# Kernel optimization log

Measured on AMD Instinct MI355X. Metric: run time of the kernel, lower is better.

Reference implementation:

```python
import jax, jax.numpy as jnp
import numpy as np

NUM_HEADS = 12


def setup_inputs() -> dict:
    key = jax.random.key(0)
    ks = jax.random.split(key, 6)
    dim = 384
    B, N = 2048, 49
    nW = 64
    return {
        "x": jax.random.normal(ks[0], (B, N, dim), dtype=jnp.float32),
        "mask": jax.random.normal(ks[1], (nW, N, N), dtype=jnp.float32),
        "qkv_w": jax.random.normal(ks[2], (3 * dim, dim), dtype=jnp.float32) * 0.02,
        "qkv_b": jax.random.normal(ks[3], (3 * dim,), dtype=jnp.float32) * 0.02,
        "proj_w": jax.random.normal(ks[4], (dim, dim), dtype=jnp.float32) * 0.02,
        "proj_b": jax.random.normal(ks[5], (dim,), dtype=jnp.float32) * 0.02,
    }


def reference(x, mask, qkv_w, qkv_b, proj_w, proj_b):
    B, N, C = x.shape
    H = NUM_HEADS
    Dh = C // H
    scale = Dh ** -0.5
    nW = mask.shape[0]

    # qkv projection: [B, N, 3C]
    qkv = x @ qkv_w.T + qkv_b
    q, k, v = jnp.split(qkv, 3, axis=-1)

    def heads(t):  # [B, N, C] -> [B, H, N, Dh]
        return t.reshape(B, N, H, Dh).transpose(0, 2, 1, 3)

    q, k, v = heads(q) * scale, heads(k), heads(v)

    # [B, H, N, N] attention scores
    attn = jnp.einsum("bhnd,bhmd->bhnm", q, k)
    # add per-window additive mask: reshape B -> (B//nW, nW)
    attn = attn.reshape(B // nW, nW, H, N, N) + mask[None, :, None, :, :]
    attn = jax.nn.softmax(attn.reshape(B, H, N, N), axis=-1)

    out = jnp.einsum("bhnm,bhmd->bhnd", attn, v)
    out = out.transpose(0, 2, 1, 3).reshape(B, N, C)
    return out @ proj_w.T + proj_b
```

## Files before the change

### kernel.cpp

```cpp
#include <hip/hip_runtime.h>
#include <hip/hip_bf16.h>
#include <stdint.h>

typedef unsigned short u16;
typedef __attribute__((ext_vector_type(8))) short short8;
typedef __attribute__((ext_vector_type(4))) short s4v;
typedef __attribute__((ext_vector_type(4))) float f32x4;

__device__ inline u16 f2bf(float f) {
    union { float f; unsigned int u; } x; x.f = f;
    unsigned int u = x.u;
    unsigned int r = (u + 0x7FFFu + ((u >> 16) & 1u)) >> 16;
    return (u16)r;
}

__device__ inline void gld_lds16(const u16* g, u16* l) {
    auto const* gp = reinterpret_cast<const __attribute__((address_space(1))) unsigned int*>(
        reinterpret_cast<uintptr_t>(g));
    auto* lp = reinterpret_cast<__attribute__((address_space(3))) unsigned int*>(
        reinterpret_cast<uintptr_t>(l));
    __builtin_amdgcn_global_load_lds(gp, lp, 16, 0, 0);
}

#if __has_builtin(__builtin_amdgcn_mfma_f32_16x16x16bf16_1k)
#define MFMA16(a, b, c) __builtin_amdgcn_mfma_f32_16x16x16bf16_1k((a), (b), (c), 0, 0, 0)
#elif __has_builtin(__builtin_amdgcn_mfma_f32_16x16x16_bf16)
#define MFMA16(a, b, c) __builtin_amdgcn_mfma_f32_16x16x16_bf16((a), (b), (c), 0, 0, 0)
#else
__device__ inline f32x4 mfma16_asm(s4v a, s4v b, f32x4 c) {
    asm volatile("s_nop 1\n\tv_mfma_f32_16x16x16_bf16 %0, %1, %2, %0\n\ts_nop 7\n\ts_nop 7"
                 : "+v"(c) : "v"(a), "v"(b));
    return c;
}
#define MFMA16(a, b, c) mfma16_asm((a), (b), (c))
#endif

#define NX8 4816896
#define NQ8 55296
#define NP8 18432
__global__ __launch_bounds__(256) void prep_all(const float* __restrict__ x,
                                                const float* __restrict__ qw,
                                                const float* __restrict__ pw,
                                                u16* __restrict__ xb,
                                                u16* __restrict__ wq,
                                                u16* __restrict__ wp) {
    size_t i = (size_t)blockIdx.x * 256 + threadIdx.x;
    const float* src; u16* dst; size_t off;
    if (i < NX8)            { src = x;  dst = xb; off = i; }
    else if (i < NX8 + NQ8) { src = qw; dst = wq; off = i - NX8; }
    else                    { src = pw; dst = wp; off = i - (NX8 + NQ8); }
    float4 v0 = ((const float4*)src)[off * 2];
    float4 v1 = ((const float4*)src)[off * 2 + 1];
    u16 h[8];
    h[0] = f2bf(v0.x); h[1] = f2bf(v0.y); h[2] = f2bf(v0.z); h[3] = f2bf(v0.w);
    h[4] = f2bf(v1.x); h[5] = f2bf(v1.y); h[6] = f2bf(v1.z); h[7] = f2bf(v1.w);
    *(uint4*)(dst + off * 8) = *(const uint4*)h;
}

__global__ __launch_bounds__(256) void qkv_gemm(const u16* __restrict__ xb,
                                                const u16* __restrict__ wq,
                                                const float* __restrict__ bias,
                                                u16* __restrict__ qkv_out) {
    __shared__ u16 As[2][128 * 32];
    __shared__ u16 Bs[2][128 * 32];
    const int tid = threadIdx.x;
    const int wave = tid >> 6, lane = tid & 63;
    const int lr = lane >> 4, lc = lane & 15;
    const int wm = (wave & 1) * 64, wn = (wave >> 1) * 64;
    const int lin = blockIdx.x;
    const int xcd = lin & 7;
    const int idx = lin >> 3;
    const int nBase = (idx % 9) * 128;
    const int mBase = (xcd * 98 + idx / 9) * 128;

    f32x4 acc[4][4] = {};

    const int srow = lane >> 2, scol = (lane & 3) * 8;
    const u16* aSrc = xb + (size_t)(mBase + wave * 32 + srow) * 384 + scol;
    const u16* bSrc = wq + (size_t)(nBase + wave * 32 + srow) * 384 + scol;

    auto stage = [&](int k0, int buf) {
        u16* aDst = &As[buf][wave * 1024];
        u16* bDst = &Bs[buf][wave * 1024];
        gld_lds16(aSrc + k0, aDst);
        gld_lds16(aSrc + k0 + (size_t)16 * 384, aDst + 512);
        gld_lds16(bSrc + k0, bDst);
        gld_lds16(bSrc + k0 + (size_t)16 * 384, bDst + 512);
    };
    auto compute = [&](int buf) {
        short8 af[4], bfr[4];
#pragma unroll
        for (int i = 0; i < 4; ++i)
            af[i] = *(const short8*)&As[buf][(wm + i * 16 + lc) * 32 + lr * 8];
#pragma unroll
        for (int j = 0; j < 4; ++j)
            bfr[j] = *(const short8*)&Bs[buf][(wn + j * 16 + lc) * 32 + lr * 8];
#pragma unroll
        for (int i = 0; i < 4; ++i)
#pragma unroll
            for (int j = 0; j < 4; ++j)
                acc[i][j] = __builtin_amdgcn_mfma_f32_16x16x32_bf16(bfr[j], af[i], acc[i][j], 0, 0, 0);
    };

    stage(0, 0);
    __syncthreads();
#pragma unroll
    for (int t = 0; t < 11; ++t) {
        stage((t + 1) * 32, (t + 1) & 1);
        compute(t & 1);
        __syncthreads();
    }
    compute(11 & 1);

    const float scale = 0.17677669529663687f;
#pragma unroll
    for (int j = 0; j < 4; ++j) {
        int gnb = nBase + wn + j * 16 + lr * 4;
        float4 bv = *(const float4*)&bias[gnb];
        float mult = (gnb < 384) ? scale : 1.0f;
#pragma unroll
        for (int i = 0; i < 4; ++i) {
            int gm = mBase + wm + i * 16 + lc;
            union { u16 h[4]; uint2 u; } pk;
            pk.h[0] = f2bf((acc[i][j][0] + bv.x) * mult);
            pk.h[1] = f2bf((acc[i][j][1] + bv.y) * mult);
            pk.h[2] = f2bf((acc[i][j][2] + bv.z) * mult);
            pk.h[3] = f2bf((acc[i][j][3] + bv.w) * mult);
            *(uint2*)(qkv_out + (size_t)gm * 1152 + gnb) = pk.u;
        }
    }
}

__global__ __launch_bounds__(256, 3) void attn_kernel(const u16* __restrict__ qkv,
                                                      const float* __restrict__ mask,
                                                      u16* __restrict__ aout) {
#define PST 68
    __shared__ u16 Vt_s[4][32 * PST];
    const int tid = threadIdx.x;
    const int wave = tid >> 6, lane = tid & 63;
    const int lr = lane >> 4, lc = lane & 15;
    const int bid = blockIdx.x;
    const int b = bid / 3;
    const int h = (bid - b * 3) * 4 + wave;
    const int w = b & 63;
    const float* mrow = mask + (size_t)w * 2401;

    const u16* Q = qkv + (size_t)b * 49 * 1152 + h * 32;
    const u16* K = Q + 384;
    const u16* V = Q + 768;

    {
        u16 vv[32];
        if (lane < 49) {
#pragma unroll
            for (int c = 0; c < 4; ++c)
                *(uint4*)&vv[c * 8] = *(const uint4*)(V + (size_t)lane * 1152 + c * 8);
        } else {
#pragma unroll
            for (int c = 0; c < 32; ++c) vv[c] = 0;
        }
#pragma unroll
        for (int d = 0; d < 32; ++d)
            Vt_s[wave][d * PST + lane] = vv[d];
    }

    short8 qf[4], kf[4];
    const short8 z8 = {0, 0, 0, 0, 0, 0, 0, 0};
#pragma unroll
    for (int i = 0; i < 4; ++i) {
        int row = i * 16 + lc;
        qf[i] = (row < 49) ? *(const short8*)(Q + (size_t)row * 1152 + lr * 8) : z8;
        kf[i] = (row < 49) ? *(const short8*)(K + (size_t)row * 1152 + lr * 8) : z8;
    }

    __syncthreads();

    s4v vfA[2][4];
#pragma unroll
    for (int nt = 0; nt < 2; ++nt)
#pragma unroll
        for (int sj = 0; sj < 4; ++sj)
            vfA[nt][sj] = *(const s4v*)&Vt_s[wave][(nt * 16 + lc) * PST + sj * 16 + lr * 4];

    f32x4 S2[4][4] = {};
#pragma unroll
    for (int si = 0; si < 4; ++si)
#pragma unroll
        for (int sj = 0; sj < 4; ++sj)
            S2[si][sj] = __builtin_amdgcn_mfma_f32_16x16x32_bf16(kf[sj], qf[si], S2[si][sj], 0, 0, 0);

    const size_t orow = (size_t)b * 49 * 384 + h * 32 + lr * 4;
#pragma unroll
    for (int si = 0; si < 4; ++si) {
        int q = si * 16 + lc;
        int im = (q < 49) ? q : 48;
        const float* mq = mrow + im * 49;
        float s = 0.0f;
        s4v pfq[4];
#pragma unroll
        for (int sj = 0; sj < 4; ++sj) {
            int kbase = sj * 16 + lr * 4;
            s4v pk;
#pragma unroll
            for (int r = 0; r < 4; ++r) {
                int k = kbase + r;
                float t = (k < 49) ? (S2[si][sj][r] + mq[k]) : -1e30f;
                float p = __expf(t);
                s += p;
                pk[r] = (short)f2bf(p);
            }
            pfq[sj] = pk;
        }
        s += __shfl_xor(s, 16);
        s += __shfl_xor(s, 32);

        f32x4 O0 = {}, O1 = {};
#pragma unroll
        for (int sj = 0; sj < 4; ++sj) {
            O0 = MFMA16(vfA[0][sj], pfq[sj], O0);
            O1 = MFMA16(vfA[1][sj], pfq[sj], O1);
        }

        if (q < 49) {
            float rl = __builtin_amdgcn_rcpf(s);
            union { u16 h[4]; uint2 u; } pk;
            pk.h[0] = f2bf(O0[0] * rl); pk.h[1] = f2bf(O0[1] * rl);
            pk.h[2] = f2bf(O0[2] * rl); pk.h[3] = f2bf(O0[3] * rl);
            *(uint2*)(aout + orow + (size_t)q * 384) = pk.u;
            pk.h[0] = f2bf(O1[0] * rl); pk.h[1] = f2bf(O1[1] * rl);
            pk.h[2] = f2bf(O1[2] * rl); pk.h[3] = f2bf(O1[3] * rl);
            *(uint2*)(aout + orow + (size_t)q * 384 + 16) = pk.u;
        }
    }
#undef PST
}

__global__ __launch_bounds__(256) void proj_gemm(const u16* __restrict__ a,
                                                 const u16* __restrict__ wp,
                                                 const float* __restrict__ bias,
                                                 float* __restrict__ out) {
    __shared__ u16 As[2][128 * 32];
    __shared__ u16 Bs[2][128 * 32];
    const int tid = threadIdx.x;
    const int wave = tid >> 6, lane = tid & 63;
    const int lr = lane >> 4, lc = lane & 15;
    const int wm = (wave & 1) * 64, wn = (wave >> 1) * 64;
    const int lin = blockIdx.x;
    const int xcd = lin & 7;
    const int idx = lin >> 3;
    const int nBase = (idx % 3) * 128;
    const int mBase = (xcd * 98 + idx / 3) * 128;

    f32x4 acc[4][4] = {};

    const int srow = lane >> 2, scol = (lane & 3) * 8;
    const u16* aSrc = a  + (size_t)(mBase + wave * 32 + srow) * 384 + scol;
    const u16* bSrc = wp + (size_t)(nBase + wave * 32 + srow) * 384 + scol;

    auto stage = [&](int k0, int buf) {
        u16* aDst = &As[buf][wave * 1024];
        u16* bDst = &Bs[buf][wave * 1024];
        gld_lds16(aSrc + k0, aDst);
        gld_lds16(aSrc + k0 + (size_t)16 * 384, aDst + 512);
        gld_lds16(bSrc + k0, bDst);
        gld_lds16(bSrc + k0 + (size_t)16 * 384, bDst + 512);
    };
    auto compute = [&](int buf) {
        short8 af[4], bfr[4];
#pragma unroll
        for (int i = 0; i < 4; ++i)
            af[i] = *(const short8*)&As[buf][(wm + i * 16 + lc) * 32 + lr * 8];
#pragma unroll
        for (int j = 0; j < 4; ++j)
            bfr[j] = *(const short8*)&Bs[buf][(wn + j * 16 + lc) * 32 + lr * 8];
#pragma unroll
        for (int i = 0; i < 4; ++i)
#pragma unroll
            for (int j = 0; j < 4; ++j)
                acc[i][j] = __builtin_amdgcn_mfma_f32_16x16x32_bf16(bfr[j], af[i], acc[i][j], 0, 0, 0);
    };

    stage(0, 0);
    __syncthreads();
#pragma unroll
    for (int t = 0; t < 11; ++t) {
        stage((t + 1) * 32, (t + 1) & 1);
        compute(t & 1);
        __syncthreads();
    }
    compute(11 & 1);

#pragma unroll
    for (int j = 0; j < 4; ++j) {
        int gnb = nBase + wn + j * 16 + lr * 4;
        float4 bv = *(const float4*)&bias[gnb];
#pragma unroll
        for (int i = 0; i < 4; ++i) {
            int gm = mBase + wm + i * 16 + lc;
            float4 o;
            o.x = acc[i][j][0] + bv.x;
            o.y = acc[i][j][1] + bv.y;
            o.z = acc[i][j][2] + bv.z;
            o.w = acc[i][j][3] + bv.w;
            *(float4*)(out + (size_t)gm * 384 + gnb) = o;
        }
    }
}

extern "C" void kernel_launch(void* const* d_in, const int* in_sizes, int n_in,
                              void* d_out, int out_size, void* d_ws, size_t ws_size,
                              hipStream_t stream) {
    const float* x      = (const float*)d_in[0];
    const float* mask   = (const float*)d_in[1];
    const float* qkv_w  = (const float*)d_in[2];
    const float* qkv_b  = (const float*)d_in[3];
    const float* proj_w = (const float*)d_in[4];
    const float* proj_b = (const float*)d_in[5];
    float* out = (float*)d_out;

    char* ws = (char*)d_ws;
    u16* wq   = (u16*)ws;
    u16* wp   = (u16*)(ws + 884736);
    u16* qkvb = (u16*)(ws + 1179648);
    u16* xb   = (u16*)(ws + 232390656);
    u16* attn = xb;

    prep_all<<<19104, 256, 0, stream>>>(x, qkv_w, proj_w, xb, wq, wp);
    qkv_gemm<<<7056, 256, 0, stream>>>(xb, wq, qkv_b, qkvb);
    attn_kernel<<<6144, 256, 0, stream>>>(qkvb, mask, attn);
    proj_gemm<<<2352, 256, 0, stream>>>(attn, wp, proj_b, out);
}
```

Before: 561.1 us.

## Fuse QKV projection and window attention into one kernel per head pair-window

Merges the QKV GEMM and the attention kernel. Each block computes Q, K and V for one head over two 49-row windows (98 rows) straight into LDS and then runs attention from LDS, so the bf16 qkv tensor never makes a round trip through global memory. The prep kernel reorders the QKV weight rows per head so each block loads a contiguous 96-row weight slice. The cost is a smaller 98-row M tile with clamped padding, six-way N fragments, and a larger LDS footprint per block.

Measured after the change: 509.2 us. 9.3% less time.

```diff
diff --git a/kernel.cpp b/kernel.cpp
--- a/kernel.cpp
+++ b/kernel.cpp
@@ -42,169 +42,164 @@
                                                 const float* __restrict__ qw,
                                                 const float* __restrict__ pw,
                                                 u16* __restrict__ xb,
-                                                u16* __restrict__ wq,
+                                                u16* __restrict__ wqr,
                                                 u16* __restrict__ wp) {
     size_t i = (size_t)blockIdx.x * 256 + threadIdx.x;
-    const float* src; u16* dst; size_t off;
-    if (i < NX8)            { src = x;  dst = xb; off = i; }
-    else if (i < NX8 + NQ8) { src = qw; dst = wq; off = i - NX8; }
-    else                    { src = pw; dst = wp; off = i - (NX8 + NQ8); }
-    float4 v0 = ((const float4*)src)[off * 2];
-    float4 v1 = ((const float4*)src)[off * 2 + 1];
+    const float* src; u16* dst; size_t soff, doff;
+    if (i < NX8) {
+        src = x; dst = xb; soff = i; doff = i;
+    } else if (i < NX8 + NQ8) {
+        size_t off = i - NX8;
+        int orow = (int)(off / 48);
+        int chunk = (int)(off - (size_t)orow * 48);
+        int sec = orow / 384;
+        int rem = orow - sec * 384;
+        int hh = rem >> 5, d = rem & 31;
+        int nrow = hh * 96 + sec * 32 + d;
+        src = qw; dst = wqr; soff = off; doff = (size_t)nrow * 48 + chunk;
+    } else {
+        src = pw; dst = wp; soff = i - (NX8 + NQ8); doff = soff;
+    }
+    float4 v0 = ((const float4*)src)[soff * 2];
+    float4 v1 = ((const float4*)src)[soff * 2 + 1];
     u16 h[8];
     h[0] = f2bf(v0.x); h[1] = f2bf(v0.y); h[2] = f2bf(v0.z); h[3] = f2bf(v0.w);
     h[4] = f2bf(v1.x); h[5] = f2bf(v1.y); h[6] = f2bf(v1.z); h[7] = f2bf(v1.w);
-    *(uint4*)(dst + off * 8) = *(const uint4*)h;
-}
-
-__global__ __launch_bounds__(256) void qkv_gemm(const u16* __restrict__ xb,
-                                                const u16* __restrict__ wq,
-                                                const float* __restrict__ bias,
-                                                u16* __restrict__ qkv_out) {
-    __shared__ u16 As[2][128 * 32];
-    __shared__ u16 Bs[2][128 * 32];
+    *(uint4*)(dst + doff * 8) = *(const uint4*)h;
+}
+
+__global__ __launch_bounds__(256, 3) void qkv_attn(const u16* __restrict__ xb,
+                                                   const u16* __restrict__ wqr,
+                                                   const float* __restrict__ bias,
+                                                   const float* __restrict__ mask,
+                                                   u16* __restrict__ aout) {
+    __shared__ __align__(16) u16 lds[14336];
+    u16* Abuf[2] = { lds, lds + 4096 };
+    u16* Bbuf[2] = { lds + 8192, lds + 11264 };
+    u16* QK = lds;
+    u16* Vt = lds + 8704;
+
     const int tid = threadIdx.x;
     const int wave = tid >> 6, lane = tid & 63;
     const int lr = lane >> 4, lc = lane & 15;
-    const int wm = (wave & 1) * 64, wn = (wave >> 1) * 64;
     const int lin = blockIdx.x;
     const int xcd = lin & 7;
     const int idx = lin >> 3;
-    const int nBase = (idx % 9) * 128;
-    const int mBase = (xcd * 98 + idx / 9) * 128;
-
-    f32x4 acc[4][4] = {};
+    const int h = idx % 12;
+    const int mp = xcd * 128 + idx / 12;
+    const int row0 = mp * 98;
+
+    f32x4 acc[2][6] = {};
 
     const int srow = lane >> 2, scol = (lane & 3) * 8;
-    const u16* aSrc = xb + (size_t)(mBase + wave * 32 + srow) * 384 + scol;
-    const u16* bSrc = wq + (size_t)(nBase + wave * 32 + srow) * 384 + scol;
+    const int ar0 = row0 + wave * 32 + srow;
+    const int ar1 = (ar0 < 100351) ? ar0 : 100351;
+    const int ar2 = (ar0 + 16 < 100351) ? ar0 + 16 : 100351;
+    const u16* aSrc1 = xb + (size_t)ar1 * 384 + scol;
+    const u16* aSrc2 = xb + (size_t)ar2 * 384 + scol;
+    const u16* bSrc = wqr + (size_t)(h * 96 + wave * 16 + srow) * 384 + scol;
 
     auto stage = [&](int k0, int buf) {
-        u16* aDst = &As[buf][wave * 1024];
-        u16* bDst = &Bs[buf][wave * 1024];
-        gld_lds16(aSrc + k0, aDst);
-        gld_lds16(aSrc + k0 + (size_t)16 * 384, aDst + 512);
-        gld_lds16(bSrc + k0, bDst);
-        gld_lds16(bSrc + k0 + (size_t)16 * 384, bDst + 512);
+        gld_lds16(aSrc1 + k0, Abuf[buf] + wave * 1024);
+        gld_lds16(aSrc2 + k0, Abuf[buf] + wave * 1024 + 512);
+        gld_lds16(bSrc + k0, Bbuf[buf] + wave * 512);
+        if (wave < 2)
+            gld_lds16(bSrc + (size_t)64 * 384 + k0, Bbuf[buf] + 2048 + wave * 512);
     };
     auto compute = [&](int buf) {
-        short8 af[4], bfr[4];
-#pragma unroll
-        for (int i = 0; i < 4; ++i)
-            af[i] = *(const short8*)&As[buf][(wm + i * 16 + lc) * 32 + lr * 8];
-#pragma unroll
-        for (int j = 0; j < 4; ++j)
-            bfr[j] = *(const short8*)&Bs[buf][(wn + j * 16 + lc) * 32 + lr * 8];
-#pragma unroll
-        for (int i = 0; i < 4; ++i)
-#pragma unroll
-            for (int j = 0; j < 4; ++j)
+        short8 af[2], bfr[6];
+#pragma unroll
+        for (int i = 0; i < 2; ++i)
+            af[i] = *(const short8*)&Abuf[buf][(wave * 32 + i * 16 + lc) * 32 + lr * 8];
+#pragma unroll
+        for (int j = 0; j < 6; ++j)
+            bfr[j] = *(const short8*)&Bbuf[buf][(j * 16 + lc) * 32 + lr * 8];
+#pragma unroll
+        for (int i = 0; i < 2; ++i)
+#pragma unroll
+            for (int j = 0; j < 6; ++j)
                 acc[i][j] = __builtin_amdgcn_mfma_f32_16x16x32_bf16(bfr[j], af[i], acc[i][j], 0, 0, 0);
     };
 
     stage(0, 0);
     __syncthreads();
 #pragma unroll
-    for (int t = 0; t < 11; ++t) {
-        stage((t + 1) * 32, (t + 1) & 1);
+    for (int t = 0; t < 12; ++t) {
+        if (t < 11) stage((t + 1) * 32, (t + 1) & 1);
         compute(t & 1);
         __syncthreads();
     }
-    compute(11 & 1);
 
     const float scale = 0.17677669529663687f;
 #pragma unroll
-    for (int j = 0; j < 4; ++j) {
-        int gnb = nBase + wn + j * 16 + lr * 4;
-        float4 bv = *(const float4*)&bias[gnb];
-        float mult = (gnb < 384) ? scale : 1.0f;
-#pragma unroll
-        for (int i = 0; i < 4; ++i) {
-            int gm = mBase + wm + i * 16 + lc;
-            union { u16 h[4]; uint2 u; } pk;
-            pk.h[0] = f2bf((acc[i][j][0] + bv.x) * mult);
-            pk.h[1] = f2bf((acc[i][j][1] + bv.y) * mult);
-            pk.h[2] = f2bf((acc[i][j][2] + bv.z) * mult);
-            pk.h[3] = f2bf((acc[i][j][3] + bv.w) * mult);
-            *(uint2*)(qkv_out + (size_t)gm * 1152 + gnb) = pk.u;
-        }
-    }
-}
-
-__global__ __launch_bounds__(256, 3) void attn_kernel(const u16* __restrict__ qkv,
-                                                      const float* __restrict__ mask,
-                                                      u16* __restrict__ aout) {
-#define PST 68
-    __shared__ u16 Vt_s[4][32 * PST];
-    const int tid = threadIdx.x;
-    const int wave = tid >> 6, lane = tid & 63;
-    const int lr = lane >> 4, lc = lane & 15;
-    const int bid = blockIdx.x;
-    const int b = bid / 3;
-    const int h = (bid - b * 3) * 4 + wave;
-    const int w = b & 63;
-    const float* mrow = mask + (size_t)w * 2401;
-
-    const u16* Q = qkv + (size_t)b * 49 * 1152 + h * 32;
-    const u16* K = Q + 384;
-    const u16* V = Q + 768;
-
-    {
-        u16 vv[32];
-        if (lane < 49) {
-#pragma unroll
-            for (int c = 0; c < 4; ++c)
-                *(uint4*)&vv[c * 8] = *(const uint4*)(V + (size_t)lane * 1152 + c * 8);
-        } else {
-#pragma unroll
-            for (int c = 0; c < 32; ++c) vv[c] = 0;
-        }
-#pragma unroll
-        for (int d = 0; d < 32; ++d)
-            Vt_s[wave][d * PST + lane] = vv[d];
-    }
-
-    short8 qf[4], kf[4];
-    const short8 z8 = {0, 0, 0, 0, 0, 0, 0, 0};
-#pragma unroll
-    for (int i = 0; i < 4; ++i) {
-        int row = i * 16 + lc;
-        qf[i] = (row < 49) ? *(const short8*)(Q + (size_t)row * 1152 + lr * 8) : z8;
-        kf[i] = (row < 49) ? *(const short8*)(K + (size_t)row * 1152 + lr * 8) : z8;
-    }
-
+    for (int j = 0; j < 6; ++j) {
+        const int sec = j >> 1;
+        const int nb = (j & 1) * 16 + lr * 4;
+        float4 bv = *(const float4*)&bias[sec * 384 + h * 32 + nb];
+        const float mult = (sec == 0) ? scale : 1.0f;
+#pragma unroll
+        for (int i = 0; i < 2; ++i) {
+            const int m = wave * 32 + i * 16 + lc;
+            float v0 = (acc[i][j][0] + bv.x) * mult;
+            float v1 = (acc[i][j][1] + bv.y) * mult;
+            float v2 = (acc[i][j][2] + bv.z) * mult;
+            float v3 = (acc[i][j][3] + bv.w) * mult;
+            if (sec < 2) {
+                union { u16 h[4]; uint2 u; } pk;
+                pk.h[0] = f2bf(v0); pk.h[1] = f2bf(v1);
+                pk.h[2] = f2bf(v2); pk.h[3] = f2bf(v3);
+                *(uint2*)&QK[m * 68 + sec * 32 + nb] = pk.u;
+            } else {
+                Vt[(nb + 0) * 132 + m] = f2bf(v0);
+                Vt[(nb + 1) * 132 + m] = f2bf(v1);
+                Vt[(nb + 2) * 132 + m] = f2bf(v2);
+                Vt[(nb + 3) * 132 + m] = f2bf(v3);
+            }
+        }
+    }
     __syncthreads();
 
+    const int winSel = wave & 1, qh = wave >> 1;
+    const int woff = winSel * 49;
+    const float* mrow = mask + (size_t)((2 * mp + winSel) & 63) * 2401;
+
+    short8 kf[4], qf[2];
     s4v vfA[2][4];
 #pragma unroll
+    for (int j = 0; j < 4; ++j)
+        kf[j] = *(const short8*)&QK[(woff + j * 16 + lc) * 68 + 32 + lr * 8];
+#pragma unroll
+    for (int ii = 0; ii < 2; ++ii)
+        qf[ii] = *(const short8*)&QK[(woff + (qh * 2 + ii) * 16 + lc) * 68 + lr * 8];
+#pragma unroll
     for (int nt = 0; nt < 2; ++nt)
 #pragma unroll
         for (int sj = 0; sj < 4; ++sj)
-            vfA[nt][sj] = *(const s4v*)&Vt_s[wave][(nt * 16 + lc) * PST + sj * 16 + lr * 4];
-
-    f32x4 S2[4][4] = {};
-#pragma unroll
-    for (int si = 0; si < 4; ++si)
+            vfA[nt][sj] = *(const s4v*)&Vt[(nt * 16 + lc) * 132 + woff + sj * 16 + lr * 4];
+
+    f32x4 S2[2][4] = {};
+#pragma unroll
+    for (int ii = 0; ii < 2; ++ii)
 #pragma unroll
         for (int sj = 0; sj < 4; ++sj)
-            S2[si][sj] = __builtin_amdgcn_mfma_f32_16x16x32_bf16(kf[sj], qf[si], S2[si][sj], 0, 0, 0);
-
-    const size_t orow = (size_t)b * 49 * 384 + h * 32 + lr * 4;
-#pragma unroll
-    for (int si = 0; si < 4; ++si) {
-        int q = si * 16 + lc;
-        int im = (q < 49) ? q : 48;
+            S2[ii][sj] = __builtin_amdgcn_mfma_f32_16x16x32_bf16(kf[sj], qf[ii], S2[ii][sj], 0, 0, 0);
+
+    const size_t orow = (size_t)(row0 + woff) * 384 + h * 32 + lr * 4;
+#pragma unroll
+    for (int ii = 0; ii < 2; ++ii) {
+        const int q = (qh * 2 + ii) * 16 + lc;
+        const int im = (q < 49) ? q : 48;
         const float* mq = mrow + im * 49;
         float s = 0.0f;
         s4v pfq[4];
 #pragma unroll
         for (int sj = 0; sj < 4; ++sj) {
-            int kbase = sj * 16 + lr * 4;
+            const int kbase = sj * 16 + lr * 4;
             s4v pk;
 #pragma unroll
             for (int r = 0; r < 4; ++r) {
-                int k = kbase + r;
-                float t = (k < 49) ? (S2[si][sj][r] + mq[k]) : -1e30f;
+                const int k = kbase + r;
+                float t = (k < 49) ? (S2[ii][sj][r] + mq[k]) : -1e30f;
                 float p = __expf(t);
                 s += p;
                 pk[r] = (short)f2bf(p);
@@ -232,7 +227,6 @@
             *(uint2*)(aout + orow + (size_t)q * 384 + 16) = pk.u;
         }
     }
-#undef PST
 }
 
 __global__ __launch_bounds__(256) void proj_gemm(const u16* __restrict__ a,
@@ -319,14 +313,12 @@
     float* out = (float*)d_out;
 
     char* ws = (char*)d_ws;
-    u16* wq   = (u16*)ws;
+    u16* wqr  = (u16*)ws;
     u16* wp   = (u16*)(ws + 884736);
-    u16* qkvb = (u16*)(ws + 1179648);
+    u16* attn = (u16*)(ws + 1179648);
     u16* xb   = (u16*)(ws + 232390656);
-    u16* attn = xb;
-
-    prep_all<<<19104, 256, 0, stream>>>(x, qkv_w, proj_w, xb, wq, wp);
-    qkv_gemm<<<7056, 256, 0, stream>>>(xb, wq, qkv_b, qkvb);
-    attn_kernel<<<6144, 256, 0, stream>>>(qkvb, mask, attn);
+
+    prep_all<<<19104, 256, 0, stream>>>(x, qkv_w, proj_w, xb, wqr, wp);
+    qkv_attn<<<12288, 256, 0, stream>>>(xb, wqr, qkv_b, mask, attn);
     proj_gemm<<<2352, 256, 0, stream>>>(attn, wp, proj_b, out);
 }
```
